# Optimization experiments

Hardware: AMD Instinct MI355X
Metric: run time of the kernel (lower is better)

## Reference

```python
import jax, jax.numpy as jnp
import numpy as np

B, T, D, H = 4, 2048, 1024, 16
DH = D // H  # 64


def setup_inputs() -> dict:
    key = jax.random.key(0)
    k1, k2, k3 = jax.random.split(key, 3)
    x = jax.random.normal(k1, (B, T, D), dtype=jnp.float32)
    w_qkv = jax.random.normal(k2, (D, 3 * D), dtype=jnp.float32) * (D ** -0.5)
    w_out = jax.random.normal(k3, (D, D), dtype=jnp.float32) * (D ** -0.5)
    return {"x": x, "w_qkv": w_qkv, "w_out": w_out}


def reference(x, w_qkv, w_out):
    b, t, d = x.shape
    qkv = jnp.einsum('btd,de->bte', x, w_qkv)  # [B,T,3D]
    q, k, v = jnp.split(qkv, 3, axis=-1)
    # [B,H,T,DH]
    q = q.reshape(b, t, H, DH).transpose(0, 2, 1, 3)
    k = k.reshape(b, t, H, DH).transpose(0, 2, 1, 3)
    v = v.reshape(b, t, H, DH).transpose(0, 2, 1, 3)
    logits = jnp.einsum('bhqd,bhkd->bhqk', q, k) * (1.0 / jnp.sqrt(jnp.float32(DH)))
    # causal bias: -inf strictly above the diagonal (key index > query index)
    causal = jnp.tril(jnp.ones((t, t), dtype=bool))
    logits = jnp.where(causal, logits, jnp.float32(-jnp.inf))
    scores = jax.nn.softmax(logits, axis=-1)
    y = jnp.einsum('bhqk,bhkd->bhqd', scores, v)
    y = y.transpose(0, 2, 1, 3).reshape(b, t, d)
    return jnp.einsum('btd,de->bte', y, w_out)
```

## Files before the change

### kernel.cpp

```cpp
#include <hip/hip_runtime.h>
#include <hip/hip_bf16.h>


namespace {
constexpr int kB = 4, kT = 2048, kD = 1024, kH = 16;
constexpr int kM = kB * kT;
constexpr int kNq = 3 * kD;
}

typedef unsigned short u16;
typedef short bf16x8 __attribute__((ext_vector_type(8)));
typedef float f32x4 __attribute__((ext_vector_type(4)));

__device__ __forceinline__ u16 f2bf(float f) {
  unsigned int u = __float_as_uint(f);
  u += 0x7fffu + ((u >> 16) & 1u);
  return (u16)(u >> 16);
}
__device__ __forceinline__ unsigned int pack2(float a, float b) {
  return (unsigned int)f2bf(a) | ((unsigned int)f2bf(b) << 16);
}

__device__ __forceinline__ void gload16(const u16* g, u16* l) {
  __builtin_amdgcn_global_load_lds(
      (const __attribute__((address_space(1))) unsigned int*)(uintptr_t)g,
      (__attribute__((address_space(3))) unsigned int*)(uintptr_t)l, 16, 0, 0);
}

__global__ __launch_bounds__(256) void cvt_bf16(const float* __restrict__ x,
                                                u16* __restrict__ xb) {
  const size_t i = ((size_t)blockIdx.x * 256 + threadIdx.x) * 8;
  const float4 v0 = *(const float4*)(x + i);
  const float4 v1 = *(const float4*)(x + i + 4);
  uint4 p;
  p.x = pack2(v0.x, v0.y);
  p.y = pack2(v0.z, v0.w);
  p.z = pack2(v1.x, v1.y);
  p.w = pack2(v1.z, v1.w);
  *(uint4*)(xb + i) = p;
}

__global__ __launch_bounds__(256) void transpose_bf(const float* __restrict__ W,
                                                    u16* __restrict__ WT,
                                                    int K, int N) {
  __shared__ float T[32][33];
  const int tid = threadIdx.x;
  const int nb = blockIdx.x * 32, kb = blockIdx.y * 32;
  const int r = tid >> 3, c = (tid & 7) * 4;
  const float4 v = *(const float4*)&W[(size_t)(kb + r) * N + nb + c];
  T[r][c + 0] = v.x;
  T[r][c + 1] = v.y;
  T[r][c + 2] = v.z;
  T[r][c + 3] = v.w;
  __syncthreads();
  uint2 p;
  p.x = pack2(T[c + 0][r], T[c + 1][r]);
  p.y = pack2(T[c + 2][r], T[c + 3][r]);
  *(uint2*)&WT[(size_t)(nb + r) * K + kb + c] = p;
}

template <bool F32OUT>
__global__ __launch_bounds__(256) void gemm_bt(const u16* __restrict__ A,
                                               const u16* __restrict__ BT,
                                               void* __restrict__ Cv, int lda,
                                               int ldc) {
  __shared__ u16 As[128 * 32];
  __shared__ u16 Bs[128 * 32];
  const int tid = threadIdx.x;
  const int w = tid >> 6, lane = tid & 63;
  const int col = lane & 15, quad = lane >> 4;
  const int wm = (w & 1) * 64, wn = (w >> 1) * 64;
  const int m0 = blockIdx.y * 128, n0 = blockIdx.x * 128;

  const int s0 = tid, s1 = 256 + tid;
  const int ar0 = s0 >> 2, ak0 = ((s0 & 3) ^ ((ar0 >> 1) & 3)) * 8;
  const int ar1 = s1 >> 2, ak1 = ((s1 & 3) ^ ((ar1 >> 1) & 3)) * 8;
  const u16* agp0 = A + (size_t)(m0 + ar0) * lda + ak0;
  const u16* agp1 = A + (size_t)(m0 + ar1) * lda + ak1;
  const u16* bgp0 = BT + (size_t)(n0 + ar0) * kD + ak0;
  const u16* bgp1 = BT + (size_t)(n0 + ar1) * kD + ak1;
  u16* al0 = &As[s0 * 8];
  u16* al1 = &As[s1 * 8];
  u16* bl0 = &Bs[s0 * 8];
  u16* bl1 = &Bs[s1 * 8];

  f32x4 acc[4][4];
#pragma unroll
  for (int mi = 0; mi < 4; ++mi)
#pragma unroll
    for (int ni = 0; ni < 4; ++ni) acc[mi][ni] = (f32x4){0.f, 0.f, 0.f, 0.f};

  for (int k0 = 0; k0 < kD; k0 += 32) {
    __syncthreads();
    gload16(agp0 + k0, al0);
    gload16(agp1 + k0, al1);
    gload16(bgp0 + k0, bl0);
    gload16(bgp1 + k0, bl1);
    __syncthreads();
    bf16x8 af[4], bfr[4];
#pragma unroll
    for (int mi = 0; mi < 4; ++mi) {
      const int r = wm + mi * 16 + col;
      af[mi] = *(const bf16x8*)&As[r * 32 + ((quad ^ ((r >> 1) & 3)) * 8)];
    }
#pragma unroll
    for (int ni = 0; ni < 4; ++ni) {
      const int r = wn + ni * 16 + col;
      bfr[ni] = *(const bf16x8*)&Bs[r * 32 + ((quad ^ ((r >> 1) & 3)) * 8)];
    }
#pragma unroll
    for (int mi = 0; mi < 4; ++mi)
#pragma unroll
      for (int ni = 0; ni < 4; ++ni)
        acc[mi][ni] = __builtin_amdgcn_mfma_f32_16x16x32_bf16(
            af[mi], bfr[ni], acc[mi][ni], 0, 0, 0);
  }

#pragma unroll
  for (int mi = 0; mi < 4; ++mi)
#pragma unroll
    for (int reg = 0; reg < 4; ++reg) {
      const int row = m0 + wm + mi * 16 + quad * 4 + reg;
#pragma unroll
      for (int ni = 0; ni < 4; ++ni) {
        const int cc = n0 + wn + ni * 16 + col;
        if (F32OUT)
          ((float*)Cv)[(size_t)row * ldc + cc] = acc[mi][ni][reg];
        else
          ((u16*)Cv)[(size_t)row * ldc + cc] = f2bf(acc[mi][ni][reg]);
      }
    }
}

__global__ __launch_bounds__(256) void attn_fwd(u16* __restrict__ qkv) {
  __shared__ u16 Ks[64][72];
  __shared__ u16 Vt[64][72];
  __shared__ u16 Ps[64][72];
  const int tid = threadIdx.x;
  const int w = tid >> 6, lane = tid & 63;
  const int col = lane & 15, quad = lane >> 4;
  const int bh = blockIdx.x;
  const int b = bh >> 4, h = bh & 15;
  const int pa = blockIdx.y;
  const size_t base = (size_t)(b * kT) * kNq + h * 64;
  constexpr float kS = 0.180336880f;

  const int vkp = (tid & 31) * 2, vd0 = (tid >> 5) * 8;
  const int krow = tid >> 2, kc0 = (tid & 3) * 16;

#pragma unroll
  for (int pass = 0; pass < 2; ++pass) {
    const int qt = pass ? (31 - pa) : pa;
    const int q0 = qt << 6;

    bf16x8 aq[2];
#pragma unroll
    for (int ks = 0; ks < 2; ++ks)
      aq[ks] = *(const bf16x8*)(qkv + base + (size_t)(q0 + w * 16 + col) * kNq +
                                ks * 32 + quad * 8);

    f32x4 o[4];
#pragma unroll
    for (int nt = 0; nt < 4; ++nt) o[nt] = (f32x4){0.f, 0.f, 0.f, 0.f};
    float l_i = 0.f;

    for (int kt = 0; kt <= qt; ++kt) {
      const int k0 = kt << 6;
      __syncthreads();
      {
        const u16* kp = qkv + base + kD + (size_t)(k0 + krow) * kNq + kc0;
        *(uint4*)&Ks[krow][kc0] = *(const uint4*)kp;
        *(uint4*)&Ks[krow][kc0 + 8] = *(const uint4*)(kp + 8);
      }
      {
        const u16* vp = qkv + base + 2 * kD + (size_t)(k0 + vkp) * kNq + vd0;
        const uint4 va = *(const uint4*)vp;
        const uint4 vb = *(const uint4*)(vp + kNq);
        const u16* pa_ = (const u16*)&va;
        const u16* pb_ = (const u16*)&vb;
#pragma unroll
        for (int i = 0; i < 8; ++i) {
          const unsigned int pk =
              (unsigned int)pa_[i] | ((unsigned int)pb_[i] << 16);
          *(unsigned int*)&Vt[vd0 + i][vkp] = pk;
        }
      }
      __syncthreads();

      f32x4 st[4];
#pragma unroll
      for (int nt = 0; nt < 4; ++nt) st[nt] = (f32x4){0.f, 0.f, 0.f, 0.f};
#pragma unroll
      for (int ks = 0; ks < 2; ++ks) {
#pragma unroll
        for (int nt = 0; nt < 4; ++nt) {
          const bf16x8 bk =
              *(const bf16x8*)&Ks[nt * 16 + col][ks * 32 + quad * 8];
          st[nt] = __builtin_amdgcn_mfma_f32_16x16x32_bf16(bk, aq[ks], st[nt],
                                                           0, 0, 0);
        }
      }

      float psum = 0.f;
      if (kt == qt) {
        const int qrel = w * 16 + col;
#pragma unroll
        for (int nt = 0; nt < 4; ++nt)
#pragma unroll
          for (int reg = 0; reg < 4; ++reg) {
            const int krel = nt * 16 + quad * 4 + reg;
            const float p =
                (krel <= qrel) ? exp2f(st[nt][reg] * kS) : 0.f;
            st[nt][reg] = p;
            psum += p;
          }
      } else {
#pragma unroll
        for (int nt = 0; nt < 4; ++nt)
#pragma unroll
          for (int reg = 0; reg < 4; ++reg) {
            const float p = exp2f(st[nt][reg] * kS);
            st[nt][reg] = p;
            psum += p;
          }
      }
      psum += __shfl_xor(psum, 16, 64);
      psum += __shfl_xor(psum, 32, 64);
      l_i += psum;

#pragma unroll
      for (int nt = 0; nt < 4; ++nt) {
        uint2 pk;
        pk.x = pack2(st[nt][0], st[nt][1]);
        pk.y = pack2(st[nt][2], st[nt][3]);
        *(uint2*)&Ps[w * 16 + col][nt * 16 + quad * 4] = pk;
      }

#pragma unroll
      for (int ks = 0; ks < 2; ++ks) {
        const bf16x8 ap =
            *(const bf16x8*)&Ps[w * 16 + col][ks * 32 + quad * 8];
#pragma unroll
        for (int nt = 0; nt < 4; ++nt) {
          const bf16x8 bv =
              *(const bf16x8*)&Vt[nt * 16 + col][ks * 32 + quad * 8];
          o[nt] = __builtin_amdgcn_mfma_f32_16x16x32_bf16(ap, bv, o[nt], 0, 0,
                                                          0);
        }
      }
    }

#pragma unroll
    for (int reg = 0; reg < 4; ++reg) {
      const float lq = __shfl(l_i, (lane & 48) | (quad * 4 + reg), 64);
      const float inv = 1.0f / lq;
      u16* yp =
          qkv + base + (size_t)(q0 + w * 16 + quad * 4 + reg) * kNq;
#pragma unroll
      for (int nt = 0; nt < 4; ++nt)
        yp[nt * 16 + col] = f2bf(o[nt][reg] * inv);
    }
  }
}

extern "C" void kernel_launch(void* const* d_in, const int* in_sizes, int n_in,
                              void* d_out, int out_size, void* d_ws,
                              size_t ws_size, hipStream_t stream) {
  const float* x = (const float*)d_in[0];
  const float* w_qkv = (const float*)d_in[1];
  const float* w_out = (const float*)d_in[2];

  u16* wqkvT = (u16*)d_ws;
  u16* woutT = wqkvT + (size_t)kNq * kD;
  u16* qkvb = woutT + (size_t)kD * kD;
  u16* xb = (u16*)d_out;

  cvt_bf16<<<kM * kD / 2048, 256, 0, stream>>>(x, xb);
  transpose_bf<<<dim3(kNq / 32, kD / 32), 256, 0, stream>>>(w_qkv, wqkvT, kD,
                                                            kNq);
  transpose_bf<<<dim3(kD / 32, kD / 32), 256, 0, stream>>>(w_out, woutT, kD,
                                                           kD);
  gemm_bt<false><<<dim3(kNq / 128, kM / 128), 256, 0, stream>>>(xb, wqkvT,
                                                                qkvb, kD, kNq);
  attn_fwd<<<dim3(kB * kH, 16), 256, 0, stream>>>(qkvb);
  gemm_bt<true><<<dim3(kD / 128, kM / 128), 256, 0, stream>>>(qkvb, woutT,
                                                              d_out, kNq, kD);
}
```

Before: 273.5 us.

## Fold softmax scale into Q weights, async K loads, faster packing

The softmax scale (log2e/sqrt(dh)) is folded into the Q columns of the transposed QKV weight, which removes a multiply per logit in attention. K tiles are now loaded with global_load_lds straight into an XOR-swizzled unpadded LDS layout instead of through registers. V transposition uses byte-permute instructions, and P is packed with the hardware v_cvt_pk_bf16_f32 instruction. Scaling Q before it is rounded to bf16 changes rounding slightly, and the no-max softmax still relies on the logits staying bounded.

```diff
diff --git a/kernel.cpp b/kernel.cpp
--- a/kernel.cpp
+++ b/kernel.cpp
@@ -6,6 +6,7 @@
 constexpr int kB = 4, kT = 2048, kD = 1024, kH = 16;
 constexpr int kM = kB * kT;
 constexpr int kNq = 3 * kD;
+constexpr float kS = 0.180336880f;
 }
 
 typedef unsigned short u16;
@@ -19,6 +20,11 @@
 }
 __device__ __forceinline__ unsigned int pack2(float a, float b) {
   return (unsigned int)f2bf(a) | ((unsigned int)f2bf(b) << 16);
+}
+__device__ __forceinline__ unsigned int cvtpk(float a, float b) {
+  unsigned int r;
+  asm("v_cvt_pk_bf16_f32 %0, %1, %2" : "=v"(r) : "v"(a), "v"(b));
+  return r;
 }
 
 __device__ __forceinline__ void gload16(const u16* g, u16* l) {
@@ -42,7 +48,7 @@
 
 __global__ __launch_bounds__(256) void transpose_bf(const float* __restrict__ W,
                                                     u16* __restrict__ WT,
-                                                    int K, int N) {
+                                                    int K, int N, int nscale) {
   __shared__ float T[32][33];
   const int tid = threadIdx.x;
   const int nb = blockIdx.x * 32, kb = blockIdx.y * 32;
@@ -53,9 +59,10 @@
   T[r][c + 2] = v.z;
   T[r][c + 3] = v.w;
   __syncthreads();
+  const float s = (nb + r < nscale) ? kS : 1.0f;
   uint2 p;
-  p.x = pack2(T[c + 0][r], T[c + 1][r]);
-  p.y = pack2(T[c + 2][r], T[c + 3][r]);
+  p.x = pack2(T[c + 0][r] * s, T[c + 1][r] * s);
+  p.y = pack2(T[c + 2][r] * s, T[c + 3][r] * s);
   *(uint2*)&WT[(size_t)(nb + r) * K + kb + c] = p;
 }
 
@@ -133,7 +140,7 @@
 }
 
 __global__ __launch_bounds__(256) void attn_fwd(u16* __restrict__ qkv) {
-  __shared__ u16 Ks[64][72];
+  __shared__ u16 Ks[64 * 64];
   __shared__ u16 Vt[64][72];
   __shared__ u16 Ps[64][72];
   const int tid = threadIdx.x;
@@ -143,10 +150,15 @@
   const int b = bh >> 4, h = bh & 15;
   const int pa = blockIdx.y;
   const size_t base = (size_t)(b * kT) * kNq + h * 64;
-  constexpr float kS = 0.180336880f;
+
+  const int krr = lane >> 3;
+  const int ksw = (lane & 7) ^ krr;
+  const u16* const kgbase =
+      qkv + base + kD + (size_t)(w * 16 + krr) * kNq + ksw * 8;
+  u16* const kl0 = &Ks[(w * 16) * 64];
+  u16* const kl1 = &Ks[(w * 16 + 8) * 64];
 
   const int vkp = (tid & 31) * 2, vd0 = (tid >> 5) * 8;
-  const int krow = tid >> 2, kc0 = (tid & 3) * 16;
 
 #pragma unroll
   for (int pass = 0; pass < 2; ++pass) {
@@ -167,22 +179,20 @@
     for (int kt = 0; kt <= qt; ++kt) {
       const int k0 = kt << 6;
       __syncthreads();
-      {
-        const u16* kp = qkv + base + kD + (size_t)(k0 + krow) * kNq + kc0;
-        *(uint4*)&Ks[krow][kc0] = *(const uint4*)kp;
-        *(uint4*)&Ks[krow][kc0 + 8] = *(const uint4*)(kp + 8);
-      }
+      gload16(kgbase + (size_t)k0 * kNq, kl0);
+      gload16(kgbase + (size_t)(k0 + 8) * kNq, kl1);
       {
         const u16* vp = qkv + base + 2 * kD + (size_t)(k0 + vkp) * kNq + vd0;
         const uint4 va = *(const uint4*)vp;
         const uint4 vb = *(const uint4*)(vp + kNq);
-        const u16* pa_ = (const u16*)&va;
-        const u16* pb_ = (const u16*)&vb;
-#pragma unroll
-        for (int i = 0; i < 8; ++i) {
-          const unsigned int pk =
-              (unsigned int)pa_[i] | ((unsigned int)pb_[i] << 16);
-          *(unsigned int*)&Vt[vd0 + i][vkp] = pk;
+        const unsigned int* aw = (const unsigned int*)&va;
+        const unsigned int* bw = (const unsigned int*)&vb;
+#pragma unroll
+        for (int i = 0; i < 4; ++i) {
+          *(unsigned int*)&Vt[vd0 + 2 * i][vkp] =
+              __builtin_amdgcn_perm(bw[i], aw[i], 0x05040100u);
+          *(unsigned int*)&Vt[vd0 + 2 * i + 1][vkp] =
+              __builtin_amdgcn_perm(bw[i], aw[i], 0x07060302u);
         }
       }
       __syncthreads();
@@ -194,8 +204,10 @@
       for (int ks = 0; ks < 2; ++ks) {
 #pragma unroll
         for (int nt = 0; nt < 4; ++nt) {
-          const bf16x8 bk =
-              *(const bf16x8*)&Ks[nt * 16 + col][ks * 32 + quad * 8];
+          const int kr = nt * 16 + col;
+          const bf16x8 bk = *(const bf16x8*)&Ks[kr * 64 +
+                                                (((ks * 4 + quad) ^ (col & 7)) *
+                                                 8)];
           st[nt] = __builtin_amdgcn_mfma_f32_16x16x32_bf16(bk, aq[ks], st[nt],
                                                            0, 0, 0);
         }
@@ -209,8 +221,7 @@
 #pragma unroll
           for (int reg = 0; reg < 4; ++reg) {
             const int krel = nt * 16 + quad * 4 + reg;
-            const float p =
-                (krel <= qrel) ? exp2f(st[nt][reg] * kS) : 0.f;
+            const float p = (krel <= qrel) ? exp2f(st[nt][reg]) : 0.f;
             st[nt][reg] = p;
             psum += p;
           }
@@ -219,7 +230,7 @@
         for (int nt = 0; nt < 4; ++nt)
 #pragma unroll
           for (int reg = 0; reg < 4; ++reg) {
-            const float p = exp2f(st[nt][reg] * kS);
+            const float p = exp2f(st[nt][reg]);
             st[nt][reg] = p;
             psum += p;
           }
@@ -231,8 +242,8 @@
 #pragma unroll
       for (int nt = 0; nt < 4; ++nt) {
         uint2 pk;
-        pk.x = pack2(st[nt][0], st[nt][1]);
-        pk.y = pack2(st[nt][2], st[nt][3]);
+        pk.x = cvtpk(st[nt][0], st[nt][1]);
+        pk.y = cvtpk(st[nt][2], st[nt][3]);
         *(uint2*)&Ps[w * 16 + col][nt * 16 + quad * 4] = pk;
       }
 
@@ -277,9 +288,9 @@
 
   cvt_bf16<<<kM * kD / 2048, 256, 0, stream>>>(x, xb);
   transpose_bf<<<dim3(kNq / 32, kD / 32), 256, 0, stream>>>(w_qkv, wqkvT, kD,
-                                                            kNq);
+                                                            kNq, kD);
   transpose_bf<<<dim3(kD / 32, kD / 32), 256, 0, stream>>>(w_out, woutT, kD,
-                                                           kD);
+                                                           kD, 0);
   gemm_bt<false><<<dim3(kNq / 128, kM / 128), 256, 0, stream>>>(xb, wqkvT,
                                                                 qkvb, kD, kNq);
   attn_fwd<<<dim3(kB * kH, 16), 256, 0, stream>>>(qkvb);
```

After: 265.9 us. -2.8%, faster.
